# Optimization experiments

Measured on AMD Instinct MI355X. Metric: run time of the kernel, lower is better.

The kernel has to match this reference:

```python
import jax, jax.numpy as jnp
import numpy as np

LARGE_CONSTANT = 1e9


def setup_inputs() -> dict:
    key = jax.random.key(0)
    ks = jax.random.split(key, 8)
    B, S, D, U = 8, 2048, 1024, 1024
    scale = 1.0 / np.sqrt(D)
    inputs_1 = jax.random.normal(ks[0], (B, S, D), dtype=jnp.float32)
    inputs_2 = jax.random.normal(ks[1], (B, S, D), dtype=jnp.float32)
    Wq = jax.random.normal(ks[2], (D, U), dtype=jnp.float32) * scale
    Wk = jax.random.normal(ks[3], (D, U), dtype=jnp.float32) * scale
    Wv = jax.random.normal(ks[4], (D, U), dtype=jnp.float32) * scale
    bq = jnp.zeros((U,), dtype=jnp.float32)
    bk = jnp.zeros((U,), dtype=jnp.float32)
    bv = jnp.zeros((U,), dtype=jnp.float32)
    # metric initialized as identity in the original; add small noise to exercise it
    metric = jnp.eye(U, dtype=jnp.float32) + 0.01 * jax.random.normal(ks[5], (U, U), dtype=jnp.float32)
    return {"inputs_1": inputs_1, "inputs_2": inputs_2, "Wq": Wq, "bq": bq,
            "Wk": Wk, "bk": bk, "Wv": Wv, "bv": bv, "metric": metric}


def reference(inputs_1, inputs_2, Wq, bq, Wk, bk, Wv, bv, metric):
    U = Wq.shape[1]
    scaling = jnp.sqrt(jnp.asarray(U, dtype=inputs_1.dtype))
    queries = inputs_1 @ Wq + bq            # [b, i, u]
    keys = inputs_2 @ Wk + bk               # [b, j, u]
    values = inputs_2 @ Wv + bv             # [b, j, u]
    queries = jnp.einsum('biu,uv->biv', queries, metric)  # learned-metric transform
    scores = jnp.einsum('biu,bju->bij', queries, keys) / scaling
    # causal mask: band_part(ones, -1, 0) is lower-triangular
    S = scores.shape[-1]
    causal = jnp.tril(jnp.ones((S, S), dtype=scores.dtype))
    scores = scores - LARGE_CONSTANT * (1.0 - causal)
    alpha = jax.nn.softmax(scores, axis=-1)
    return jnp.einsum('bij,bju->biu', alpha, values)
```

## Files before the change

kernel.cpp:

```cpp
#include <hip/hip_runtime.h>


#define Bq 8
#define Sq 2048
#define Dq 1024
#define Uq 1024

typedef __bf16 bf16;
typedef __bf16 bf16x8 __attribute__((ext_vector_type(8)));
typedef float f32x4 __attribute__((ext_vector_type(4)));
typedef unsigned short u16;
typedef unsigned int u32;

__device__ __forceinline__ u16 f2bf(float f) {
  u32 u = __builtin_bit_cast(u32, f);
  u32 r = u + 0x7fffu + ((u >> 16) & 1u);
  return (u16)(r >> 16);
}
__device__ __forceinline__ float bf2f(u32 h) {
  return __builtin_bit_cast(float, h << 16);
}

__device__ __forceinline__ void gl_lds16(const void* g, void* l) {
  __builtin_amdgcn_global_load_lds(
      (const __attribute__((address_space(1))) u32*)g,
      (__attribute__((address_space(3))) u32*)l, 16, 0, 0);
}


__global__ __launch_bounds__(256) void cvt_x(const float* __restrict__ x1,
                                             const float* __restrict__ x2,
                                             u16* __restrict__ o1,
                                             u16* __restrict__ o2, int n4) {
  int idx = blockIdx.x * 256 + threadIdx.x;
  if (idx >= n4) return;
  const float* in = blockIdx.y ? x2 : x1;
  u16* out = blockIdx.y ? o2 : o1;
  float4 v = ((const float4*)in)[idx];
  ushort4 o;
  o.x = f2bf(v.x); o.y = f2bf(v.y); o.z = f2bf(v.z); o.w = f2bf(v.w);
  ((ushort4*)out)[idx] = o;
}

__global__ __launch_bounds__(256) void cvt_bf16(const float* __restrict__ in,
                                                u16* __restrict__ out, int n4) {
  int idx = blockIdx.x * 256 + threadIdx.x;
  if (idx >= n4) return;
  float4 v = ((const float4*)in)[idx];
  ushort4 o;
  o.x = f2bf(v.x); o.y = f2bf(v.y); o.z = f2bf(v.z); o.w = f2bf(v.w);
  ((ushort4*)out)[idx] = o;
}

__global__ __launch_bounds__(256) void transpose_cvt3(
    const float* __restrict__ s0, u16* __restrict__ d0,
    const float* __restrict__ s1, u16* __restrict__ d1,
    const float* __restrict__ s2, u16* __restrict__ d2) {
  __shared__ float tile[32][33];
  const float* in = (blockIdx.z == 0) ? s0 : (blockIdx.z == 1) ? s1 : s2;
  u16* out = (blockIdx.z == 0) ? d0 : (blockIdx.z == 1) ? d1 : d2;
  const int N = 1024;
  int tx = threadIdx.x & 31, ty = threadIdx.x >> 5;
  int x0 = blockIdx.x * 32, y0 = blockIdx.y * 32;
#pragma unroll
  for (int r = 0; r < 32; r += 8)
    tile[ty + r][tx] = in[(size_t)(y0 + ty + r) * N + x0 + tx];
  __syncthreads();
#pragma unroll
  for (int r = 0; r < 32; r += 8)
    out[(size_t)(x0 + ty + r) * N + y0 + tx] = f2bf(tile[tx][ty + r]);
}

__global__ __launch_bounds__(256) void bqm_kernel(const float* __restrict__ bq,
                                                  const float* __restrict__ metric,
                                                  float* __restrict__ bqm) {
  int v = blockIdx.x * 256 + threadIdx.x;
  float s = 0.f;
  for (int u = 0; u < Uq; ++u) s += bq[u] * metric[(size_t)u * Uq + v];
  bqm[v] = s;
}

__global__ __launch_bounds__(256) void fill_zero(float4* __restrict__ p, int n4) {
  int i = blockIdx.x * 256 + threadIdx.x;
  if (i < n4) p[i] = float4{0.f, 0.f, 0.f, 0.f};
}

#define BM 128
#define BN 128
#define BK 32

template <int OUT_BF16, int BIAS>
__global__ __launch_bounds__(256) void gemm_tn(
    const bf16* __restrict__ A, const bf16* __restrict__ B, void* __restrict__ Cv,
    const float* __restrict__ bias, int lda, int ldb, int ldc,
    long long sA, long long sB, long long sC, int K,
    int causal_skip, int causal_klimit) {
  __shared__ __align__(16) bf16 lA[3][BM * BK];
  __shared__ __align__(16) bf16 lB[3][BN * BK];
  int bx = causal_klimit ? (gridDim.x - 1 - blockIdx.x) : blockIdx.x;
  int m0 = bx * BM, n0 = blockIdx.y * BN;
  if (causal_skip && n0 > m0 + BM - 1) return;
  long long b = blockIdx.z;
  A += b * sA;
  B += b * sB;
  int t = threadIdx.x;
  int w = t >> 6, l = t & 63;
  int wr = (w >> 1) * 64, wc = (w & 1) * 64;
  int Kend = causal_klimit ? min(K, m0 + BM) : K;
  int nk = Kend / BK;

  f32x4 acc[4][4] = {};
  int rowA = t >> 2, kc = (t & 3) * 8;
  int lm = l & 15, q = l >> 4;

  const bf16* gA = A + (long long)(m0 + rowA) * lda + kc;
  const bf16* gB = B + (long long)(n0 + rowA) * ldb + kc;
  long long a64 = (long long)64 * lda, b64 = (long long)64 * ldb;

  auto stage = [&](int kt, int buf) {
    int k0 = kt * BK;
    char* dA = (char*)lA[buf] + w * 1024;
    char* dB = (char*)lB[buf] + w * 1024;
    gl_lds16(gA + k0, dA);
    gl_lds16(gA + k0 + a64, dA + 4096);
    gl_lds16(gB + k0, dB);
    gl_lds16(gB + k0 + b64, dB + 4096);
  };

  stage(0, 0);
  stage(1, 1);
  int cur = 0;
  for (int kt = 0; kt < nk; ++kt) {
    if (kt + 2 < nk) {
      int pb = cur + 2;
      if (pb >= 3) pb -= 3;
      stage(kt + 2, pb);
      asm volatile("s_waitcnt vmcnt(8)\n\ts_barrier" ::: "memory");
    } else if (kt + 1 < nk) {
      asm volatile("s_waitcnt vmcnt(4)\n\ts_barrier" ::: "memory");
    } else {
      asm volatile("s_waitcnt vmcnt(0)\n\ts_barrier" ::: "memory");
    }
    bf16x8 af[4], bfr[4];
#pragma unroll
    for (int i = 0; i < 4; ++i)
      af[i] = *(const bf16x8*)&lA[cur][(wr + i * 16 + lm) * BK + q * 8];
#pragma unroll
    for (int i = 0; i < 4; ++i)
      bfr[i] = *(const bf16x8*)&lB[cur][(wc + i * 16 + lm) * BK + q * 8];
#pragma unroll
    for (int i = 0; i < 4; ++i)
#pragma unroll
      for (int j = 0; j < 4; ++j)
        acc[i][j] = __builtin_amdgcn_mfma_f32_16x16x32_bf16(af[i], bfr[j], acc[i][j], 0, 0, 0);
    asm volatile("s_barrier" ::: "memory");
    cur = (cur == 2) ? 0 : cur + 1;
  }

  char* Cb = (char*)Cv + (OUT_BF16 ? b * sC * 2 : b * sC * 4);
#pragma unroll
  for (int i = 0; i < 4; ++i) {
#pragma unroll
    for (int j = 0; j < 4; ++j) {
      int col = n0 + wc + j * 16 + lm;
      float bc = (BIAS == 1) ? bias[col] : 0.f;
#pragma unroll
      for (int r = 0; r < 4; ++r) {
        int row = m0 + wr + i * 16 + q * 4 + r;
        float v = acc[i][j][r] + bc;
        if (BIAS == 2) v += bias[row];
        size_t idx = (size_t)row * ldc + col;
        if (OUT_BF16)
          ((u16*)Cb)[idx] = f2bf(v);
        else
          ((float*)Cb)[idx] = v;
      }
    }
  }
}

__global__ __launch_bounds__(256) void softmax_causal(u16* __restrict__ sc) {
  __shared__ __align__(16) float sm[Sq];
  __shared__ float red[8];
  int gr = blockIdx.x;
  int i = gr & (Sq - 1);
  u16* rowp = sc + (size_t)gr * Sq;
  int t = threadIdx.x;
  uint4 pk = ((const uint4*)rowp)[t];
  float4 lo, hi;
  lo.x = bf2f(pk.x & 0xffffu); lo.y = bf2f(pk.x >> 16);
  lo.z = bf2f(pk.y & 0xffffu); lo.w = bf2f(pk.y >> 16);
  hi.x = bf2f(pk.z & 0xffffu); hi.y = bf2f(pk.z >> 16);
  hi.z = bf2f(pk.w & 0xffffu); hi.w = bf2f(pk.w >> 16);
  ((float4*)sm)[2 * t] = lo;
  ((float4*)sm)[2 * t + 1] = hi;
  __syncthreads();
  int nv = i + 1;
  const float scl = 0.03125f;
  float m = -1e30f;
  for (int j = t; j < nv; j += 256) m = fmaxf(m, sm[j]);
#pragma unroll
  for (int o = 32; o; o >>= 1) m = fmaxf(m, __shfl_xor(m, o));
  if ((t & 63) == 0) red[t >> 6] = m;
  __syncthreads();
  m = fmaxf(fmaxf(red[0], red[1]), fmaxf(red[2], red[3])) * scl;
  float sum = 0.f;
  for (int j = t; j < nv; j += 256) sum += __expf(sm[j] * scl - m);
#pragma unroll
  for (int o = 32; o; o >>= 1) sum += __shfl_xor(sum, o);
  if ((t & 63) == 0) red[4 + (t >> 6)] = sum;
  __syncthreads();
  float rinv = 1.0f / (red[4] + red[5] + red[6] + red[7]);
  int j0 = t * 8;
  u16 ov[8];
#pragma unroll
  for (int k = 0; k < 8; ++k)
    ov[k] = (j0 + k < nv) ? f2bf(__expf(sm[j0 + k] * scl - m) * rinv) : (u16)0;
  uint4 po;
  po.x = (u32)ov[0] | ((u32)ov[1] << 16);
  po.y = (u32)ov[2] | ((u32)ov[3] << 16);
  po.z = (u32)ov[4] | ((u32)ov[5] << 16);
  po.w = (u32)ov[6] | ((u32)ov[7] << 16);
  ((uint4*)rowp)[t] = po;
}


extern "C" void kernel_launch(void* const* d_in, const int* in_sizes, int n_in,
                              void* d_out, int out_size, void* d_ws, size_t ws_size,
                              hipStream_t stream) {
  const float* X1 = (const float*)d_in[0];
  const float* X2 = (const float*)d_in[1];
  const float* Wq = (const float*)d_in[2];
  const float* bq = (const float*)d_in[3];
  const float* Wk = (const float*)d_in[4];
  const float* bk = (const float*)d_in[5];
  const float* Wv = (const float*)d_in[6];
  const float* bv = (const float*)d_in[7];
  const float* metric = (const float*)d_in[8];
  float* out = (float*)d_out;

  const size_t XB = (size_t)Bq * Sq * Dq * 2;
  const size_t WB = (size_t)Dq * Uq * 2;
  const size_t NEED = 3 * XB + 5 * WB + 4096;

  if (ws_size < NEED) {
    fill_zero<<<(out_size / 4 + 255) / 256, 256, 0, stream>>>((float4*)d_out, out_size / 4);
    return;
  }

  char* ws = (char*)d_ws;
  bf16* X1b = (bf16*)(ws);
  bf16* X2b = (bf16*)(ws + XB);
  bf16* Vt = (bf16*)(ws + 2 * XB);
  bf16* WqB = (bf16*)(ws + 3 * XB);
  bf16* metT = (bf16*)(ws + 3 * XB + WB);
  bf16* WkT = (bf16*)(ws + 3 * XB + 2 * WB);
  bf16* WvT = (bf16*)(ws + 3 * XB + 3 * WB);
  bf16* WqmT = (bf16*)(ws + 3 * XB + 4 * WB);
  float* bqm = (float*)(ws + 3 * XB + 5 * WB);
  u16* Sc = (u16*)ws;
  bf16* Qb = (bf16*)d_out;
  bf16* Kb = (bf16*)d_out + (size_t)Bq * Sq * Uq;

  int nx4 = Bq * Sq * Dq / 4;
  cvt_x<<<dim3((nx4 + 255) / 256, 2), 256, 0, stream>>>(X1, X2, (u16*)X1b, (u16*)X2b, nx4);
  cvt_bf16<<<(Dq * Uq / 4 + 255) / 256, 256, 0, stream>>>(Wq, (u16*)WqB, Dq * Uq / 4);
  transpose_cvt3<<<dim3(32, 32, 3), 256, 0, stream>>>(
      metric, (u16*)metT, Wk, (u16*)WkT, Wv, (u16*)WvT);
  bqm_kernel<<<Uq / 256, 256, 0, stream>>>(bq, metric, bqm);

  gemm_tn<1, 0><<<dim3(Uq / BM, Dq / BN, 1), 256, 0, stream>>>(
      metT, WqB, WqmT, nullptr, Uq, Uq, Dq, 0, 0, 0, Uq, 0, 0);

  const int MQ = Bq * Sq;
  gemm_tn<1, 1><<<dim3(MQ / BM, Uq / BN, 1), 256, 0, stream>>>(
      X1b, WqmT, Qb, bqm, Dq, Dq, Uq, 0, 0, 0, Dq, 0, 0);
  gemm_tn<1, 1><<<dim3(MQ / BM, Uq / BN, 1), 256, 0, stream>>>(
      X2b, WkT, Kb, bk, Dq, Dq, Uq, 0, 0, 0, Dq, 0, 0);
  gemm_tn<1, 2><<<dim3(Uq / BM, Sq / BN, Bq), 256, 0, stream>>>(
      WvT, X2b, Vt, bv, Dq, Dq, Sq, 0, (long long)Sq * Dq, (long long)Uq * Sq, Dq, 0, 0);

  gemm_tn<1, 0><<<dim3(Sq / BM, Sq / BN, Bq), 256, 0, stream>>>(
      Qb, Kb, Sc, nullptr, Uq, Uq, Sq, (long long)Sq * Uq, (long long)Sq * Uq,
      (long long)Sq * Sq, Uq, 1, 0);

  softmax_causal<<<Bq * Sq, 256, 0, stream>>>(Sc);

  gemm_tn<0, 0><<<dim3(Sq / BM, Uq / BN, Bq), 256, 0, stream>>>(
      (const bf16*)Sc, Vt, out, nullptr, Sq, Sq, Uq, (long long)Sq * Sq,
      (long long)Uq * Sq, (long long)Sq * Uq, Sq, 0, 1);

  (void)in_sizes; (void)n_in; (void)ws_size;
}
```

Measured before the change: 600.9 us.

## Load B operand fragments directly from global into registers, bypassing LDS

The B tile is no longer staged through shared memory. Each wave loads its B MFMA fragments straight from global memory into registers, double-buffered across a K loop unrolled by two, while A keeps its triple-buffered LDS pipeline. This cuts LDS footprint and LDS traffic, which may raise occupancy, but B fragments are now loaded redundantly by the two waves that share columns, with less coalesced access. The vmcnt counts are hand-tuned to a mix of A and B loads, and the unroll by two assumes nk is even.

After: 798.7 us. 1.33x slower.

```diff
diff --git a/kernel.cpp b/kernel.cpp
--- a/kernel.cpp
+++ b/kernel.cpp
@@ -96,7 +96,6 @@
     long long sA, long long sB, long long sC, int K,
     int causal_skip, int causal_klimit) {
   __shared__ __align__(16) bf16 lA[3][BM * BK];
-  __shared__ __align__(16) bf16 lB[3][BN * BK];
   int bx = causal_klimit ? (gridDim.x - 1 - blockIdx.x) : blockIdx.x;
   int m0 = bx * BM, n0 = blockIdx.y * BN;
   if (causal_skip && n0 > m0 + BM - 1) return;
@@ -114,45 +113,58 @@
   int lm = l & 15, q = l >> 4;
 
   const bf16* gA = A + (long long)(m0 + rowA) * lda + kc;
-  const bf16* gB = B + (long long)(n0 + rowA) * ldb + kc;
-  long long a64 = (long long)64 * lda, b64 = (long long)64 * ldb;
-
-  auto stage = [&](int kt, int buf) {
-    int k0 = kt * BK;
+  long long a64 = (long long)64 * lda;
+  const bf16* gBbase = B + (long long)(n0 + wc + lm) * ldb + q * 8;
+  long long b16 = (long long)16 * ldb;
+
+  auto stageA = [&](int kt, int buf) {
     char* dA = (char*)lA[buf] + w * 1024;
-    char* dB = (char*)lB[buf] + w * 1024;
-    gl_lds16(gA + k0, dA);
-    gl_lds16(gA + k0 + a64, dA + 4096);
-    gl_lds16(gB + k0, dB);
-    gl_lds16(gB + k0 + b64, dB + 4096);
+    gl_lds16(gA + kt * BK, dA);
+    gl_lds16(gA + kt * BK + a64, dA + 4096);
   };
-
-  stage(0, 0);
-  stage(1, 1);
+  bf16x8 bA[4], bB[4];
+  auto loadB = [&](int kt, bf16x8* bf) {
+    const bf16* p = gBbase + kt * BK;
+#pragma unroll
+    for (int j = 0; j < 4; ++j) bf[j] = *(const bf16x8*)(p + j * b16);
+  };
+  auto compute = [&](int buf, bf16x8* bf) {
+    bf16x8 af[4];
+#pragma unroll
+    for (int i = 0; i < 4; ++i)
+      af[i] = *(const bf16x8*)&lA[buf][(wr + i * 16 + lm) * BK + q * 8];
+#pragma unroll
+    for (int i = 0; i < 4; ++i)
+#pragma unroll
+      for (int j = 0; j < 4; ++j)
+        acc[i][j] = __builtin_amdgcn_mfma_f32_16x16x32_bf16(af[i], bf[j], acc[i][j], 0, 0, 0);
+  };
+
+  loadB(0, bA);
+  stageA(0, 0);
+  stageA(1, 1);
   int cur = 0;
-  for (int kt = 0; kt < nk; ++kt) {
+  for (int kt = 0; kt < nk; kt += 2) {
+    loadB(kt + 1, bB);
     if (kt + 2 < nk) {
-      int pb = cur + 2;
-      if (pb >= 3) pb -= 3;
-      stage(kt + 2, pb);
+      int pb = cur + 2; if (pb >= 3) pb -= 3;
+      stageA(kt + 2, pb);
       asm volatile("s_waitcnt vmcnt(8)\n\ts_barrier" ::: "memory");
-    } else if (kt + 1 < nk) {
-      asm volatile("s_waitcnt vmcnt(4)\n\ts_barrier" ::: "memory");
+    } else {
+      asm volatile("s_waitcnt vmcnt(6)\n\ts_barrier" ::: "memory");
+    }
+    compute(cur, bA);
+    asm volatile("s_barrier" ::: "memory");
+    cur = (cur == 2) ? 0 : cur + 1;
+    if (kt + 2 < nk) loadB(kt + 2, bA);
+    if (kt + 3 < nk) {
+      int pb = cur + 2; if (pb >= 3) pb -= 3;
+      stageA(kt + 3, pb);
+      asm volatile("s_waitcnt vmcnt(8)\n\ts_barrier" ::: "memory");
     } else {
       asm volatile("s_waitcnt vmcnt(0)\n\ts_barrier" ::: "memory");
     }
-    bf16x8 af[4], bfr[4];
-#pragma unroll
-    for (int i = 0; i < 4; ++i)
-      af[i] = *(const bf16x8*)&lA[cur][(wr + i * 16 + lm) * BK + q * 8];
-#pragma unroll
-    for (int i = 0; i < 4; ++i)
-      bfr[i] = *(const bf16x8*)&lB[cur][(wc + i * 16 + lm) * BK + q * 8];
-#pragma unroll
-    for (int i = 0; i < 4; ++i)
-#pragma unroll
-      for (int j = 0; j < 4; ++j)
-        acc[i][j] = __builtin_amdgcn_mfma_f32_16x16x32_bf16(af[i], bfr[j], acc[i][j], 0, 0, 0);
+    compute(cur, bB);
     asm volatile("s_barrier" ::: "memory");
     cur = (cur == 2) ? 0 : cur + 1;
   }
```
